# Optimization experiments

Hardware: AMD Instinct MI355X
Metric: run time of the kernel (lower is better)

The kernel has to match this reference:

```python
import jax, jax.numpy as jnp
import numpy as np

BETA = 1.0 - 0.01      # 1 - voltage_decay
THRESH = 1.0           # threshold_voltage; theta state is never updated in the
                       # original forward (theta1/theta2 stay at init=0), so the
                       # effective adaptive threshold is THRESH + 0 every step.
ALPHA = 2.0            # snntorch default ATan surrogate alpha

@jax.custom_vjp
def spike_fn(x):
    # Heaviside forward, ATan surrogate backward (snntorch default spike_grad)
    return (x > 0).astype(x.dtype)

def _spike_fwd(x):
    return (x > 0).astype(x.dtype), x

def _spike_bwd(x, g):
    return (g * (ALPHA / 2.0) / (1.0 + (jnp.pi / 2.0 * ALPHA * x) ** 2),)

spike_fn.defvjp(_spike_fwd, _spike_bwd)

def setup_inputs() -> dict:
    key = jax.random.key(0)
    k0, k1, k2 = jax.random.split(key, 3)
    B, T, D, H, A = 128, 32, 6400, 1000, 4
    x = jax.random.normal(k0, (B, T, D), jnp.float32)
    W1 = jax.random.normal(k1, (H, D), jnp.float32) * (1.0 / np.sqrt(D))
    b1 = jnp.zeros((H,), jnp.float32)
    W2 = jax.random.normal(k2, (A, H), jnp.float32) * (1.0 / np.sqrt(H))
    b2 = jnp.zeros((A,), jnp.float32)
    return {"x": x, "W1": W1, "b1": b1, "W2": W2, "b2": b2}

def _lif_step(mem, cur, thr):
    # snntorch Leaky, reset_mechanism='zero':
    #   reset based on PREVIOUS mem crossing threshold (detached),
    #   zeroes the whole new state (leaked mem + input) on reset step.
    reset = jax.lax.stop_gradient((mem > thr).astype(mem.dtype))
    mem_new = (BETA * mem + cur) * (1.0 - reset)
    spk = spike_fn(mem_new - thr)
    return spk, mem_new

def _snn_forward(x, W1, b1, W2, b2):
    B, T, _ = x.shape
    H, A = W1.shape[0], W2.shape[0]

    def step(carry, cur):
        mem1, mem2 = carry
        h1 = cur @ W1.T + b1                 # [B,H]
        spk1, mem1 = _lif_step(mem1, h1, THRESH)
        h2 = spk1 @ W2.T + b2                # [B,A]
        spk2, mem2 = _lif_step(mem2, h2, THRESH)
        return (mem1, mem2), spk2

    init = (jnp.zeros((B, H), x.dtype), jnp.zeros((B, A), x.dtype))
    xt = jnp.swapaxes(x, 0, 1)               # [T,B,D]
    _, spk2_rec = jax.lax.scan(step, init, xt)
    return jnp.swapaxes(spk2_rec, 0, 1)      # [B,T,A]

def reference(x, W1, b1, W2, b2):
    return _snn_forward(x, W1, b1, W2, b2)
```

## Files before the change

kernel.cpp:

```cpp
#include <hip/hip_runtime.h>
#include <hip/hip_bf16.h>

constexpr int Bn = 128;
constexpr int Tn = 32;
constexpr int Dn = 6400;
constexpr int Hn = 1000;
constexpr int An = 4;
constexpr int Mn = Bn * Tn;
constexpr int Npad = 1024;

constexpr int KS = Dn / 32;
constexpr int MC = Mn / 16;
constexpr int NC = Npad / 16;

typedef _Float16 half8 __attribute__((ext_vector_type(8)));
typedef _Float16 half4 __attribute__((ext_vector_type(4)));
typedef float floatx4 __attribute__((ext_vector_type(4)));

constexpr size_t H1_BYTES  = (size_t)Mn * Hn * 4;
constexpr size_t XS_BYTES  = (size_t)Mn * Dn * 2;
constexpr size_t WSp_BYTES = (size_t)Npad * Dn * 2;
constexpr size_t WS_R7     = H1_BYTES + 2 * XS_BYTES + 2 * WSp_BYTES;
constexpr size_t WS_SPLITK = 2 * H1_BYTES + 2 * XS_BYTES + 2 * WSp_BYTES;

__device__ __forceinline__ void async16(const void* g, void* l) {
    __builtin_amdgcn_global_load_lds(
        (const __attribute__((address_space(1))) void*)g,
        (__attribute__((address_space(3))) void*)l, 16, 0, 0);
}

__global__ __launch_bounds__(256)
void cvt2(const float* __restrict__ X, const float* __restrict__ W1,
          _Float16* __restrict__ Xh, _Float16* __restrict__ Xl,
          _Float16* __restrict__ Wh, _Float16* __restrict__ Wl)
{
    constexpr int LD2 = 264;
    __shared__ __align__(16) _Float16 hiS[16][LD2];
    __shared__ __align__(16) _Float16 loS[16][LD2];

    const int tid = threadIdx.x;
    const int lane = tid & 63;
    const int w = tid >> 6;
    const int bx = blockIdx.x;

    const float* src;
    _Float16 *dh, *dl;
    int c4, ks0, crow, nrows;
    if (bx < 256 * 25) {
        c4 = bx & 255; ks0 = (bx >> 8) * 8;
        src = X; dh = Xh; dl = Xl; crow = MC; nrows = 16;
    } else {
        const int b2 = bx - 256 * 25;
        c4 = b2 & 63; ks0 = (b2 >> 6) * 8;
        src = W1; dh = Wh; dl = Wl; crow = NC; nrows = Hn - c4 * 16;
    }

#pragma unroll
    for (int j = 0; j < 4; ++j) {
        const int row = w * 4 + j;
        float4 v = make_float4(0.f, 0.f, 0.f, 0.f);
        if (row < nrows)
            v = *(const float4*)(src + (size_t)(c4 * 16 + row) * Dn + ks0 * 32 + lane * 4);
        half4 hi, lo;
        const float vx = v.x * 16.0f, vy = v.y * 16.0f,
                    vz = v.z * 16.0f, vw = v.w * 16.0f;
        hi[0] = (_Float16)vx; lo[0] = (_Float16)(vx - (float)hi[0]);
        hi[1] = (_Float16)vy; lo[1] = (_Float16)(vy - (float)hi[1]);
        hi[2] = (_Float16)vz; lo[2] = (_Float16)(vz - (float)hi[2]);
        hi[3] = (_Float16)vw; lo[3] = (_Float16)(vw - (float)hi[3]);
        *(half4*)&hiS[row][lane * 4] = hi;
        *(half4*)&loS[row][lane * 4] = lo;
    }
    __syncthreads();

    const int lr = lane & 15, lg = lane >> 4;
#pragma unroll
    for (int q = 0; q < 2; ++q) {
        const int ks = w * 2 + q;
        const size_t cbase = ((size_t)(ks0 + ks) * crow + c4) * 512;
        const half8 h = *(const half8*)&hiS[lr][ks * 32 + lg * 8];
        const half8 l = *(const half8*)&loS[lr][ks * 32 + lg * 8];
        *(half8*)(dh + cbase + lane * 8) = h;
        *(half8*)(dl + cbase + lane * 8) = l;
    }
}

__global__ __launch_bounds__(256, 2)
void gemm_sk2(const _Float16* __restrict__ Xh, const _Float16* __restrict__ Xl,
              const _Float16* __restrict__ Wh, const _Float16* __restrict__ Wl,
              float* __restrict__ H1)
{
    __shared__ __align__(16) _Float16 S[4][16][512];

    const int tid = threadIdx.x;
    const int lane = tid & 63;
    const int w = tid >> 6;
    const int kh = blockIdx.x & 1;
    const int nb = (blockIdx.x >> 1) & 7;
    const int mb = blockIdx.x >> 4;
    const int bm8 = mb * 8;
    const int bn8 = nb * 8;
    const int wm = w & 1;
    const int wn = w >> 1;
    const int ks0 = kh * (KS / 2);
    constexpr int NIT = KS / 2;

    auto issueA = [&](int ks, int buf) {
        _Float16* base = &S[buf][0][0];
#pragma unroll
        for (int r = 0; r < 2; ++r) {
            const int i = w * 2 + r;
            const size_t ga = ((size_t)(ks * MC + bm8 + i)) * 512 + lane * 8;
            async16(Xh + ga, base + (0 + i) * 512);
            async16(Xl + ga, base + (8 + i) * 512);
        }
    };

    const _Float16* bhp = Wh + ((size_t)(ks0 * NC + bn8 + wn * 4)) * 512 + lane * 8;
    const _Float16* blp = Wl + ((size_t)(ks0 * NC + bn8 + wn * 4)) * 512 + lane * 8;
    constexpr size_t BSTEP = (size_t)NC * 512;

    floatx4 acc[4][4] = {};

    half8 bhA[4], blA[4], bhB[4], blB[4];

    issueA(ks0 + 0, 0);
#pragma unroll
    for (int nt = 0; nt < 4; ++nt) {
        bhA[nt] = *(const half8*)(bhp + nt * 512);
        blA[nt] = *(const half8*)(blp + nt * 512);
    }
    issueA(ks0 + 1, 1);

#define SK2_BODY(IT, BUF, BCH, BCL, BNH, BNL)                                   \
    {                                                                           \
        asm volatile("s_waitcnt vmcnt(8)" ::: "memory");                        \
        __builtin_amdgcn_sched_barrier(0);                                      \
        __builtin_amdgcn_s_barrier();                                           \
        __builtin_amdgcn_sched_barrier(0);                                      \
        if ((IT) + 1 < NIT) {                                                   \
            const size_t bo = (size_t)((IT) + 1) * BSTEP;                       \
            _Pragma("unroll")                                                   \
            for (int nt = 0; nt < 4; ++nt) {                                    \
                BNH[nt] = *(const half8*)(bhp + bo + nt * 512);                 \
                BNL[nt] = *(const half8*)(blp + bo + nt * 512);                 \
            }                                                                   \
        }                                                                       \
        __builtin_amdgcn_sched_barrier(0);                                      \
        if ((IT) + 2 < NIT) issueA(ks0 + (IT) + 2, ((IT) + 2) & 3);             \
        __builtin_amdgcn_sched_barrier(0);                                      \
        half8 ah[4], al[4];                                                     \
        _Pragma("unroll")                                                       \
        for (int mt = 0; mt < 4; ++mt) {                                        \
            ah[mt] = *(const half8*)&S[BUF][wm * 4 + mt][lane * 8];             \
            al[mt] = *(const half8*)&S[BUF][8 + wm * 4 + mt][lane * 8];         \
        }                                                                       \
        _Pragma("unroll")                                                       \
        for (int mt = 0; mt < 4; ++mt)                                          \
            _Pragma("unroll")                                                   \
            for (int nt = 0; nt < 4; ++nt)                                      \
                acc[mt][nt] = __builtin_amdgcn_mfma_f32_16x16x32_f16(ah[mt], BCH[nt], acc[mt][nt], 0, 0, 0); \
        _Pragma("unroll")                                                       \
        for (int mt = 0; mt < 4; ++mt)                                          \
            _Pragma("unroll")                                                   \
            for (int nt = 0; nt < 4; ++nt)                                      \
                acc[mt][nt] = __builtin_amdgcn_mfma_f32_16x16x32_f16(ah[mt], BCL[nt], acc[mt][nt], 0, 0, 0); \
        _Pragma("unroll")                                                       \
        for (int mt = 0; mt < 4; ++mt)                                          \
            _Pragma("unroll")                                                   \
            for (int nt = 0; nt < 4; ++nt)                                      \
                acc[mt][nt] = __builtin_amdgcn_mfma_f32_16x16x32_f16(al[mt], BCH[nt], acc[mt][nt], 0, 0, 0); \
    }

    for (int it = 0; it < NIT; it += 4) {
        SK2_BODY(it + 0, 0, bhA, blA, bhB, blB);
        SK2_BODY(it + 1, 1, bhB, blB, bhA, blA);
        SK2_BODY(it + 2, 2, bhA, blA, bhB, blB);
        SK2_BODY(it + 3, 3, bhB, blB, bhA, blA);
    }
#undef SK2_BODY

    float* H1o = H1 + (size_t)kh * ((size_t)Mn * Hn);
    const int fr = lane & 15;
    const int fq = lane >> 4;
#pragma unroll
    for (int nt = 0; nt < 4; ++nt) {
        const int n = nb * 128 + wn * 64 + nt * 16 + fr;
        if (n >= Hn) continue;
#pragma unroll
        for (int mt = 0; mt < 4; ++mt) {
            const int m = mb * 128 + wm * 64 + mt * 16 + fq * 4;
#pragma unroll
            for (int r = 0; r < 4; ++r)
                H1o[(size_t)(m + r) * Hn + n] = acc[mt][nt][r] * (1.0f / 256.0f);
        }
    }
}

constexpr int AH = 0;
constexpr int AL = 8 * 512;
constexpr int BH = 16 * 512;
constexpr int BL = 20 * 512;
constexpr int BUFSZ = 24 * 512;

__global__ __launch_bounds__(256, 2)
void gemm_frag2(const _Float16* __restrict__ Xh, const _Float16* __restrict__ Xl,
                const _Float16* __restrict__ Wh, const _Float16* __restrict__ Wl,
                float* __restrict__ H1)
{
    __shared__ __align__(16) _Float16 S[2 * BUFSZ];

    const int tid = threadIdx.x;
    const int lane = tid & 63;
    const int w = tid >> 6;
    const int nb = blockIdx.x & 15;
    const int mb = blockIdx.x >> 4;
    const int bm4 = mb * 8;
    const int bn4 = nb * 4;
    const int wm = w & 1;
    const int wn = w >> 1;

    auto issue = [&](int ks, int buf) {
        _Float16* base = &S[buf * BUFSZ];
#pragma unroll
        for (int r = 0; r < 2; ++r) {
            const int i = w * 2 + r;
            const size_t ga = ((size_t)(ks * MC + bm4 + i)) * 512 + lane * 8;
            async16(Xh + ga, base + AH + i * 512);
            async16(Xl + ga, base + AL + i * 512);
        }
        const size_t gb = ((size_t)(ks * NC + bn4 + w)) * 512 + lane * 8;
        async16(Wh + gb, base + BH + w * 512);
        async16(Wl + gb, base + BL + w * 512);
    };

    floatx4 acc0[4][2] = {};
    floatx4 acc1[4][2] = {};

    issue(0, 0);
    for (int it = 0; it < KS; ++it) {
        const int buf = it & 1;
        __syncthreads();
        if (it + 1 < KS) issue(it + 1, buf ^ 1);

        const _Float16* base = &S[buf * BUFSZ];
        half8 ah[4], al[4], bh[2], bl[2];
#pragma unroll
        for (int mt = 0; mt < 4; ++mt) {
            ah[mt] = *(const half8*)(base + AH + (wm * 4 + mt) * 512 + lane * 8);
            al[mt] = *(const half8*)(base + AL + (wm * 4 + mt) * 512 + lane * 8);
        }
#pragma unroll
        for (int nt = 0; nt < 2; ++nt) {
            bh[nt] = *(const half8*)(base + BH + (wn * 2 + nt) * 512 + lane * 8);
            bl[nt] = *(const half8*)(base + BL + (wn * 2 + nt) * 512 + lane * 8);
        }
#pragma unroll
        for (int mt = 0; mt < 4; ++mt)
#pragma unroll
            for (int nt = 0; nt < 2; ++nt) {
                acc0[mt][nt] = __builtin_amdgcn_mfma_f32_16x16x32_f16(ah[mt], bh[nt], acc0[mt][nt], 0, 0, 0);
                acc1[mt][nt] = __builtin_amdgcn_mfma_f32_16x16x32_f16(ah[mt], bl[nt], acc1[mt][nt], 0, 0, 0);
                acc1[mt][nt] = __builtin_amdgcn_mfma_f32_16x16x32_f16(al[mt], bh[nt], acc1[mt][nt], 0, 0, 0);
            }
    }

    const int fr = lane & 15;
    const int fq = lane >> 4;
#pragma unroll
    for (int nt = 0; nt < 2; ++nt) {
        const int n = nb * 64 + wn * 32 + nt * 16 + fr;
        if (n >= Hn) continue;
#pragma unroll
        for (int mt = 0; mt < 4; ++mt) {
            const int m = mb * 128 + wm * 64 + mt * 16 + fq * 4;
#pragma unroll
            for (int r = 0; r < 4; ++r)
                H1[(size_t)(m + r) * Hn + n] =
                    (acc0[mt][nt][r] + acc1[mt][nt][r]) * (1.0f / 256.0f);
        }
    }
}

__global__ __launch_bounds__(256, 4)
void gemm_fb(const float* __restrict__ X, const float* __restrict__ W1,
             float* __restrict__ H1)
{
    constexpr int K = Dn;
    constexpr int LD = 72;
    __shared__ __align__(16) _Float16 As[2][64][LD];
    __shared__ __align__(16) _Float16 Bs[2][64][LD];

    const int tid = threadIdx.x;
    const int bm = blockIdx.x * 64;
    const int bn = blockIdx.y * 64;
    const int lane = tid & 63;
    const int wid = tid >> 6;
    const int wm = (wid & 1) * 32;
    const int wn = (wid >> 1) * 32;
    const int fr = lane & 15;
    const int fq = lane >> 4;

    const int row0 = tid >> 3;
    const int row1 = (tid + 256) >> 3;
    const int k8_0 = (tid & 7) * 8;

    float4 rx[2][2], rw[2][2];
    const float zero4[4] = {0.f, 0.f, 0.f, 0.f};

    auto load_tiles = [&](int k0) {
        rx[0][0] = *(const float4*)(X + (size_t)(bm + row0) * K + k0 + k8_0);
        rx[0][1] = *(const float4*)(X + (size_t)(bm + row0) * K + k0 + k8_0 + 4);
        rx[1][0] = *(const float4*)(X + (size_t)(bm + row1) * K + k0 + k8_0);
        rx[1][1] = *(const float4*)(X + (size_t)(bm + row1) * K + k0 + k8_0 + 4);
        const int n0 = bn + row0, n1 = bn + row1;
        if (n0 < Hn) {
            rw[0][0] = *(const float4*)(W1 + (size_t)n0 * K + k0 + k8_0);
            rw[0][1] = *(const float4*)(W1 + (size_t)n0 * K + k0 + k8_0 + 4);
        } else { rw[0][0] = *(const float4*)zero4; rw[0][1] = *(const float4*)zero4; }
        if (n1 < Hn) {
            rw[1][0] = *(const float4*)(W1 + (size_t)n1 * K + k0 + k8_0);
            rw[1][1] = *(const float4*)(W1 + (size_t)n1 * K + k0 + k8_0 + 4);
        } else { rw[1][0] = *(const float4*)zero4; rw[1][1] = *(const float4*)zero4; }
    };

    load_tiles(0);
    floatx4 acc0[2][2] = {};
    floatx4 acc1[2][2] = {};

    for (int k0 = 0; k0 < K; k0 += 64) {
#pragma unroll
        for (int p = 0; p < 2; ++p) {
            const int row = p ? row1 : row0;
            float v[8];
            *(float4*)&v[0] = rx[p][0]; *(float4*)&v[4] = rx[p][1];
            half8 hi, lo;
#pragma unroll
            for (int j = 0; j < 8; ++j) {
                hi[j] = (_Float16)v[j];
                lo[j] = (_Float16)((v[j] - (float)hi[j]) * 4096.0f);
            }
            *(half8*)&As[0][row][k8_0] = hi;
            *(half8*)&As[1][row][k8_0] = lo;

            *(float4*)&v[0] = rw[p][0]; *(float4*)&v[4] = rw[p][1];
#pragma unroll
            for (int j = 0; j < 8; ++j) {
                hi[j] = (_Float16)v[j];
                lo[j] = (_Float16)((v[j] - (float)hi[j]) * 4096.0f);
            }
            *(half8*)&Bs[0][row][k8_0] = hi;
            *(half8*)&Bs[1][row][k8_0] = lo;
        }
        __syncthreads();
        if (k0 + 64 < K) load_tiles(k0 + 64);

#pragma unroll
        for (int c = 0; c < 2; ++c) {
            half8 ahi[2], alo[2], bhi[2], blo[2];
#pragma unroll
            for (int mt = 0; mt < 2; ++mt) {
                ahi[mt] = *(const half8*)&As[0][wm + mt * 16 + fr][c * 32 + fq * 8];
                alo[mt] = *(const half8*)&As[1][wm + mt * 16 + fr][c * 32 + fq * 8];
            }
#pragma unroll
            for (int nt = 0; nt < 2; ++nt) {
                bhi[nt] = *(const half8*)&Bs[0][wn + nt * 16 + fr][c * 32 + fq * 8];
                blo[nt] = *(const half8*)&Bs[1][wn + nt * 16 + fr][c * 32 + fq * 8];
            }
#pragma unroll
            for (int mt = 0; mt < 2; ++mt)
#pragma unroll
                for (int nt = 0; nt < 2; ++nt) {
                    acc0[mt][nt] = __builtin_amdgcn_mfma_f32_16x16x32_f16(ahi[mt], bhi[nt], acc0[mt][nt], 0, 0, 0);
                    acc1[mt][nt] = __builtin_amdgcn_mfma_f32_16x16x32_f16(ahi[mt], blo[nt], acc1[mt][nt], 0, 0, 0);
                    acc1[mt][nt] = __builtin_amdgcn_mfma_f32_16x16x32_f16(alo[mt], bhi[nt], acc1[mt][nt], 0, 0, 0);
                }
        }
        __syncthreads();
    }

#pragma unroll
    for (int nt = 0; nt < 2; ++nt) {
        const int n = bn + wn + nt * 16 + fr;
        if (n >= Hn) continue;
#pragma unroll
        for (int mt = 0; mt < 2; ++mt) {
            const int m = bm + wm + mt * 16 + fq * 4;
#pragma unroll
            for (int r = 0; r < 4; ++r)
                H1[(size_t)(m + r) * Hn + n] =
                    acc0[mt][nt][r] + acc1[mt][nt][r] * (1.0f / 4096.0f);
        }
    }
}

__global__ __launch_bounds__(1024)
void snn_scan(const float* __restrict__ H1, const float* __restrict__ b1,
              const float* __restrict__ W2, const float* __restrict__ b2,
              float* __restrict__ out, int split)
{
    const int b = blockIdx.x;
    const int tid = threadIdx.x;
    const int lane = tid & 63;
    const int wid = tid >> 6;
    const bool act = (tid < Hn);
    constexpr size_t MH = (size_t)Mn * Hn;

    __shared__ float w2s[1024][5];
    __shared__ unsigned smask[1024];
    __shared__ float h2s[Tn][An];

#pragma unroll
    for (int a = 0; a < An; ++a)
        w2s[tid][a] = act ? W2[a * Hn + tid] : 0.f;

    const float b1v = act ? b1[tid] : 0.f;

    float cur[Tn];
#pragma unroll
    for (int t = 0; t < Tn; ++t) {
        const size_t idx = ((size_t)b * Tn + t) * Hn + tid;
        float c = act ? H1[idx] : 0.f;
        if (split && act) c += H1[idx + MH];
        cur[t] = c + b1v;
    }

    unsigned mask = 0;
    float mem1 = 0.f;
#pragma unroll
    for (int t = 0; t < Tn; ++t) {
        const float reset = (mem1 > 1.0f) ? 1.0f : 0.0f;
        mem1 = (0.99f * mem1 + cur[t]) * (1.0f - reset);
        if (mem1 > 1.0f) mask |= (1u << t);
    }
    smask[tid] = act ? mask : 0u;
    __syncthreads();

#pragma unroll
    for (int tt = 0; tt < 2; ++tt) {
        const int t = wid * 2 + tt;
        float p[An] = {0.f, 0.f, 0.f, 0.f};
        for (int h = lane; h < 1024; h += 64) {
            const float g = (smask[h] >> t) & 1u ? 1.0f : 0.0f;
#pragma unroll
            for (int a = 0; a < An; ++a) p[a] += g * w2s[h][a];
        }
#pragma unroll
        for (int off = 32; off > 0; off >>= 1)
#pragma unroll
            for (int a = 0; a < An; ++a) p[a] += __shfl_down(p[a], off, 64);
        if (lane == 0) {
#pragma unroll
            for (int a = 0; a < An; ++a) h2s[t][a] = p[a];
        }
    }
    __syncthreads();

    if (tid < An) {
        const float bias = b2[tid];
        float mem2 = 0.f;
#pragma unroll
        for (int t = 0; t < Tn; ++t) {
            const float h2 = h2s[t][tid] + bias;
            const float reset = (mem2 > 1.0f) ? 1.0f : 0.0f;
            mem2 = (0.99f * mem2 + h2) * (1.0f - reset);
            out[((size_t)b * Tn + t) * An + tid] = (mem2 > 1.0f) ? 1.0f : 0.0f;
        }
    }
}

extern "C" void kernel_launch(void* const* d_in, const int* in_sizes, int n_in,
                              void* d_out, int out_size, void* d_ws, size_t ws_size,
                              hipStream_t stream) {
    const float* x  = (const float*)d_in[0];
    const float* W1 = (const float*)d_in[1];
    const float* b1 = (const float*)d_in[2];
    const float* W2 = (const float*)d_in[3];
    const float* b2 = (const float*)d_in[4];
    float* out = (float*)d_out;

    char* ws = (char*)d_ws;
    float* H1 = (float*)ws;

    if (ws_size >= WS_SPLITK) {
        _Float16* Xh = (_Float16*)(ws + 2 * H1_BYTES);
        _Float16* Xl = (_Float16*)(ws + 2 * H1_BYTES + XS_BYTES);
        _Float16* Wh = (_Float16*)(ws + 2 * H1_BYTES + 2 * XS_BYTES);
        _Float16* Wl = (_Float16*)(ws + 2 * H1_BYTES + 2 * XS_BYTES + WSp_BYTES);

        cvt2<<<256 * 25 + 64 * 25, 256, 0, stream>>>(x, W1, Xh, Xl, Wh, Wl);
        gemm_sk2<<<512, 256, 0, stream>>>(Xh, Xl, Wh, Wl, H1);
        snn_scan<<<Bn, 1024, 0, stream>>>(H1, b1, W2, b2, out, 1);
    } else if (ws_size >= WS_R7) {
        _Float16* Xh = (_Float16*)(ws + H1_BYTES);
        _Float16* Xl = (_Float16*)(ws + H1_BYTES + XS_BYTES);
        _Float16* Wh = (_Float16*)(ws + H1_BYTES + 2 * XS_BYTES);
        _Float16* Wl = (_Float16*)(ws + H1_BYTES + 2 * XS_BYTES + WSp_BYTES);

        cvt2<<<256 * 25 + 64 * 25, 256, 0, stream>>>(x, W1, Xh, Xl, Wh, Wl);
        gemm_frag2<<<512, 256, 0, stream>>>(Xh, Xl, Wh, Wl, H1);
        snn_scan<<<Bn, 1024, 0, stream>>>(H1, b1, W2, b2, out, 0);
    } else {
        dim3 grid(Mn / 64, (Hn + 63) / 64);
        gemm_fb<<<grid, 256, 0, stream>>>(x, W1, H1);
        snn_scan<<<Bn, 1024, 0, stream>>>(H1, b1, W2, b2, out, 0);
    }
}
```

Before: 354.4 us.

## Stage W1 fragments through LDS with double-buffered async loads in split-K GEMM

The split-K GEMM now loads the W (B operand) tiles into shared memory with the same async copies used for X, instead of each wave reading its B fragments from global memory into registers. The A pipeline is cut from four buffers with prefetch depth two to two buffers with depth one, and each step waits for all outstanding loads. The goal is to share B tiles between the waves that use them, cutting redundant global reads and register pressure. The cost is less latency hiding, since every iteration now waits on vmcnt(0). The scan kernel's split-sum loop is also generalised to a variable number of partial sums.

```diff
diff --git a/kernel.cpp b/kernel.cpp
--- a/kernel.cpp
+++ b/kernel.cpp
@@ -86,11 +86,11 @@
 }
 
 __global__ __launch_bounds__(256, 2)
-void gemm_sk2(const _Float16* __restrict__ Xh, const _Float16* __restrict__ Xl,
-              const _Float16* __restrict__ Wh, const _Float16* __restrict__ Wl,
-              float* __restrict__ H1)
+void gemm_sk2b(const _Float16* __restrict__ Xh, const _Float16* __restrict__ Xl,
+               const _Float16* __restrict__ Wh, const _Float16* __restrict__ Wl,
+               float* __restrict__ H1)
 {
-    __shared__ __align__(16) _Float16 S[4][16][512];
+    __shared__ __align__(16) _Float16 S[2][32][512];
 
     const int tid = threadIdx.x;
     const int lane = tid & 63;
@@ -105,7 +105,7 @@
     const int ks0 = kh * (KS / 2);
     constexpr int NIT = KS / 2;
 
-    auto issueA = [&](int ks, int buf) {
+    auto issueAB = [&](int ks, int buf) {
         _Float16* base = &S[buf][0][0];
 #pragma unroll
         for (int r = 0; r < 2; ++r) {
@@ -113,72 +113,57 @@
             const size_t ga = ((size_t)(ks * MC + bm8 + i)) * 512 + lane * 8;
             async16(Xh + ga, base + (0 + i) * 512);
             async16(Xl + ga, base + (8 + i) * 512);
+            const size_t gb = ((size_t)(ks * NC + bn8 + i)) * 512 + lane * 8;
+            async16(Wh + gb, base + (16 + i) * 512);
+            async16(Wl + gb, base + (24 + i) * 512);
         }
     };
 
-    const _Float16* bhp = Wh + ((size_t)(ks0 * NC + bn8 + wn * 4)) * 512 + lane * 8;
-    const _Float16* blp = Wl + ((size_t)(ks0 * NC + bn8 + wn * 4)) * 512 + lane * 8;
-    constexpr size_t BSTEP = (size_t)NC * 512;
-
     floatx4 acc[4][4] = {};
 
-    half8 bhA[4], blA[4], bhB[4], blB[4];
-
-    issueA(ks0 + 0, 0);
-#pragma unroll
-    for (int nt = 0; nt < 4; ++nt) {
-        bhA[nt] = *(const half8*)(bhp + nt * 512);
-        blA[nt] = *(const half8*)(blp + nt * 512);
-    }
-    issueA(ks0 + 1, 1);
-
-#define SK2_BODY(IT, BUF, BCH, BCL, BNH, BNL)                                   \
+    issueAB(ks0 + 0, 0);
+
+#define SK2B_BODY(IT, BUF)                                                      \
     {                                                                           \
-        asm volatile("s_waitcnt vmcnt(8)" ::: "memory");                        \
+        asm volatile("s_waitcnt vmcnt(0)" ::: "memory");                        \
         __builtin_amdgcn_sched_barrier(0);                                      \
         __builtin_amdgcn_s_barrier();                                           \
         __builtin_amdgcn_sched_barrier(0);                                      \
-        if ((IT) + 1 < NIT) {                                                   \
-            const size_t bo = (size_t)((IT) + 1) * BSTEP;                       \
-            _Pragma("unroll")                                                   \
-            for (int nt = 0; nt < 4; ++nt) {                                    \
-                BNH[nt] = *(const half8*)(bhp + bo + nt * 512);                 \
-                BNL[nt] = *(const half8*)(blp + bo + nt * 512);                 \
-            }                                                                   \
-        }                                                                       \
+        if ((IT) + 1 < NIT) issueAB(ks0 + (IT) + 1, (BUF) ^ 1);                 \
         __builtin_amdgcn_sched_barrier(0);                                      \
-        if ((IT) + 2 < NIT) issueA(ks0 + (IT) + 2, ((IT) + 2) & 3);             \
-        __builtin_amdgcn_sched_barrier(0);                                      \
-        half8 ah[4], al[4];                                                     \
+        half8 ah[4], al[4], bh[4], bl[4];                                       \
         _Pragma("unroll")                                                       \
         for (int mt = 0; mt < 4; ++mt) {                                        \
-            ah[mt] = *(const half8*)&S[BUF][wm * 4 + mt][lane * 8];             \
+            ah[mt] = *(const half8*)&S[BUF][0 + wm * 4 + mt][lane * 8];         \
             al[mt] = *(const half8*)&S[BUF][8 + wm * 4 + mt][lane * 8];         \
+        }                                                                       \
+        _Pragma("unroll")                                                       \
+        for (int nt = 0; nt < 4; ++nt) {                                        \
+            bh[nt] = *(const half8*)&S[BUF][16 + wn * 4 + nt][lane * 8];        \
+            bl[nt] = *(const half8*)&S[BUF][24 + wn * 4 + nt][lane * 8];        \
         }                                                                       \
         _Pragma("unroll")                                                       \
         for (int mt = 0; mt < 4; ++mt)                                          \
             _Pragma("unroll")                                                   \
             for (int nt = 0; nt < 4; ++nt)                                      \
-                acc[mt][nt] = __builtin_amdgcn_mfma_f32_16x16x32_f16(ah[mt], BCH[nt], acc[mt][nt], 0, 0, 0); \
+                acc[mt][nt] = __builtin_amdgcn_mfma_f32_16x16x32_f16(ah[mt], bh[nt], acc[mt][nt], 0, 0, 0); \
         _Pragma("unroll")                                                       \
         for (int mt = 0; mt < 4; ++mt)                                          \
             _Pragma("unroll")                                                   \
             for (int nt = 0; nt < 4; ++nt)                                      \
-                acc[mt][nt] = __builtin_amdgcn_mfma_f32_16x16x32_f16(ah[mt], BCL[nt], acc[mt][nt], 0, 0, 0); \
+                acc[mt][nt] = __builtin_amdgcn_mfma_f32_16x16x32_f16(ah[mt], bl[nt], acc[mt][nt], 0, 0, 0); \
         _Pragma("unroll")                                                       \
         for (int mt = 0; mt < 4; ++mt)                                          \
             _Pragma("unroll")                                                   \
             for (int nt = 0; nt < 4; ++nt)                                      \
-                acc[mt][nt] = __builtin_amdgcn_mfma_f32_16x16x32_f16(al[mt], BCH[nt], acc[mt][nt], 0, 0, 0); \
-    }
-
-    for (int it = 0; it < NIT; it += 4) {
-        SK2_BODY(it + 0, 0, bhA, blA, bhB, blB);
-        SK2_BODY(it + 1, 1, bhB, blB, bhA, blA);
-        SK2_BODY(it + 2, 2, bhA, blA, bhB, blB);
-        SK2_BODY(it + 3, 3, bhB, blB, bhA, blA);
-    }
-#undef SK2_BODY
+                acc[mt][nt] = __builtin_amdgcn_mfma_f32_16x16x32_f16(al[mt], bh[nt], acc[mt][nt], 0, 0, 0); \
+    }
+
+    for (int it = 0; it < NIT; it += 2) {
+        SK2B_BODY(it + 0, 0);
+        SK2B_BODY(it + 1, 1);
+    }
+#undef SK2B_BODY
 
     float* H1o = H1 + (size_t)kh * ((size_t)Mn * Hn);
     const int fr = lane & 15;
@@ -422,7 +407,8 @@
     for (int t = 0; t < Tn; ++t) {
         const size_t idx = ((size_t)b * Tn + t) * Hn + tid;
         float c = act ? H1[idx] : 0.f;
-        if (split && act) c += H1[idx + MH];
+        if (act)
+            for (int s = 1; s <= split; ++s) c += H1[idx + (size_t)s * MH];
         cur[t] = c + b1v;
     }
 
@@ -490,7 +476,7 @@
         _Float16* Wl = (_Float16*)(ws + 2 * H1_BYTES + 2 * XS_BYTES + WSp_BYTES);
 
         cvt2<<<256 * 25 + 64 * 25, 256, 0, stream>>>(x, W1, Xh, Xl, Wh, Wl);
-        gemm_sk2<<<512, 256, 0, stream>>>(Xh, Xl, Wh, Wl, H1);
+        gemm_sk2b<<<512, 256, 0, stream>>>(Xh, Xl, Wh, Wl, H1);
         snn_scan<<<Bn, 1024, 0, stream>>>(H1, b1, W2, b2, out, 1);
     } else if (ws_size >= WS_R7) {
         _Float16* Xh = (_Float16*)(ws + H1_BYTES);
```

After: 345.0 us. 2.7% less time.
